# Kernel optimization log

Measured on AMD Instinct MI355X. Metric: run time of the kernel, lower is better.

Reference implementation:

```python
import jax, jax.numpy as jnp
import numpy as np
import math
from jax import lax

KSIZE = 3
STRIDE = 1
RATE = 2
FUSE_K = 3
SCALE = 10.0
FUSE = True


def extract_image_patches(img, kernel, stride=1):
    # Faithful port of the torch helper (incl. pad_row applied to width).
    bsz, c, h, w = img.shape
    h2 = math.ceil(h / stride)
    w2 = math.ceil(w / stride)
    pad_row = (h2 - 1) * stride + kernel - h
    pad_col = (w2 - 1) * stride + kernel - w
    x = jnp.pad(img, ((0, 0), (0, 0),
                      (pad_col // 2, pad_col - pad_col // 2),
                      (pad_row // 2, pad_row - pad_row // 2)))
    H, W = x.shape[2], x.shape[3]
    nh = (H - kernel) // stride + 1
    nw = (W - kernel) // stride + 1
    parts = [x[:, :, ki:ki + (nh - 1) * stride + 1:stride,
                     kj:kj + (nw - 1) * stride + 1:stride]
             for ki in range(kernel) for kj in range(kernel)]
    p = jnp.stack(parts, axis=1)  # [b, k*k, c, nh, nw] -> flatten order (ki,kj,c)
    return p.reshape(bsz, kernel * kernel * c, nh, nw)


def setup_inputs() -> dict:
    key = jax.random.key(0)
    k1, k2 = jax.random.split(key)
    f = jax.random.normal(k1, (2, 64, 128, 128), dtype=jnp.float32)
    b = jax.random.normal(k2, (2, 64, 128, 128), dtype=jnp.float32)
    mask = jnp.zeros((2, 1, 128, 128), dtype=jnp.float32)
    return {"f": f, "b": b, "mask": mask}


def reference(f, b, mask):
    kernel = RATE * 2
    bs, cs, hs, ws = f.shape
    # raw background patches at stride=rate with kernel=2*rate
    raw_w = extract_image_patches(b, kernel, RATE * STRIDE)
    raw_w = raw_w.reshape(bs, -1, kernel, kernel, cs).transpose(0, 1, 4, 2, 3)  # [bs,L,cs,K,K]
    # nearest-neighbor downsample by rate (torch nearest: src = dst*rate)
    f_ds = f[:, :, ::RATE, ::RATE]
    b_ds = b[:, :, ::RATE, ::RATE]
    mask_ds = mask[:, :, ::RATE, ::RATE]
    ihs, iws = b_ds.shape[2], b_ds.shape[3]
    L = ihs * iws
    # ksize x ksize matching patches
    w = extract_image_patches(b_ds, KSIZE, STRIDE)
    w = w.reshape(bs, -1, KSIZE, KSIZE, cs).transpose(0, 1, 4, 2, 3)  # [bs,L,cs,3,3]
    # mask patches -> per-patch validity mm [L]
    m = extract_image_patches(mask_ds, KSIZE, STRIDE)
    m = m.reshape(bs, -1, KSIZE, KSIZE, 1).transpose(0, 2, 3, 4, 1)[0]  # [3,3,1,L]
    mm = (jnp.mean(m, axis=(0, 1, 2)) == 0.0).astype(f.dtype)  # [L]
    fuse_weight = jnp.eye(FUSE_K, dtype=f.dtype).reshape(1, 1, FUSE_K, FUSE_K)

    def per_sample(xi, wi, raw_wi):
        # xi [cs,ihs,iws], wi [L,cs,3,3], raw_wi [L,cs,K,K]
        norm = jnp.sqrt(jnp.sum(wi * wi, axis=(1, 2, 3)))
        wi_normed = wi / jnp.minimum(norm, 1e-4)[:, None, None, None]  # clamp(max=1e-4), faithful
        yi = lax.conv_general_dilated(xi[None], wi_normed, (1, 1), [(1, 1), (1, 1)])  # [1,L,ihs,iws]
        if FUSE:
            yi = yi.reshape(1, 1, ihs * iws, ihs * iws)
            yi = lax.conv_general_dilated(yi, fuse_weight, (1, 1), [(1, 1), (1, 1)])
            yi = yi.reshape(1, ihs, iws, ihs, iws).transpose(0, 2, 1, 4, 3)
            yi = yi.reshape(1, 1, ihs * iws, ihs * iws)
            yi = lax.conv_general_dilated(yi, fuse_weight, (1, 1), [(1, 1), (1, 1)])
            yi = yi.reshape(1, iws, ihs, iws, ihs).transpose(0, 2, 1, 4, 3)
        yi = yi.reshape(1, ihs, iws, iws * ihs)
        yi = jax.nn.softmax(yi * mm * SCALE, axis=3) * mm
        offset = jnp.argmax(yi, axis=3).astype(jnp.int32)
        offset = jnp.stack([offset // hs, offset % hs], axis=-1).transpose(0, 3, 1, 2)  # [1,2,ihs,iws]
        yi_t = yi.transpose(0, 3, 1, 2)  # [1,L,ihs,iws]
        # conv_transpose2d(yi_t, raw_wi, stride=rate, padding=1) via lhs dilation
        w_t = jnp.flip(raw_wi, axis=(-2, -1)).transpose(1, 0, 2, 3)  # [cs,L,K,K]
        pad = kernel - 1 - 1
        out = lax.conv_general_dilated(yi_t, w_t, (1, 1), [(pad, pad), (pad, pad)],
                                       lhs_dilation=(RATE, RATE)) / 4.0  # [1,cs,hs,ws]
        return out[0], offset[0]

    y, offsets = jax.vmap(per_sample)(f_ds, w, raw_w)
    h_add = jnp.broadcast_to(jnp.arange(ihs, dtype=offsets.dtype).reshape(1, 1, ihs, 1), (bs, 1, ihs, iws))
    w_add = jnp.broadcast_to(jnp.arange(iws, dtype=offsets.dtype).reshape(1, 1, 1, iws), (bs, 1, ihs, iws))
    offsets = offsets - jnp.concatenate([h_add, w_add], axis=1)
    return y, offsets
```

## Files before the change

kernel.cpp:

```cpp
#include <hip/hip_runtime.h>
#include <math.h>

#define NS   4096
#define KCH  576
#define CH   64
#define HF   128
#define HD   64
#define PLANE (NS*KCH)

typedef __attribute__((ext_vector_type(8))) _Float16 half8;
typedef __attribute__((ext_vector_type(4))) float f32x4;

__device__ __forceinline__ int Tsw(int r){ return ((r & 63) << 6) | (r >> 6); }

typedef __attribute__((address_space(1))) unsigned int gu32;
typedef __attribute__((address_space(3))) unsigned int lu32;
__device__ __forceinline__ void gload16(const void* g, void* l){
  __builtin_amdgcn_global_load_lds((const gu32*)g, (lu32*)l, 16, 0, 0);
}

__global__ void k_mm(const float* __restrict__ mask, float* __restrict__ mm){
  int n = blockIdx.x * blockDim.x + threadIdx.x;
  if(n >= NS) return;
  float sum = 0.f;
  #pragma unroll
  for(int r9 = 0; r9 < 9; ++r9){
    int idx = n * 9 + r9;
    int p   = idx >> 12;
    int rem = idx & 4095;
    int y = rem >> 6, x = rem & 63;
    int ki = p / 3, kj = p % 3;
    int Y = ki + y - 1, X = kj + x - 1;
    float v = 0.f;
    if(Y >= 0 && Y < HD && X >= 0 && X < HD)
      v = mask[(2*Y) * HF + 2*X];
    sum += v;
  }
  mm[n] = ((sum / 9.0f) == 0.0f) ? 1.0f : 0.0f;
}

__global__ void k_WX(const float* __restrict__ fp, const float* __restrict__ bp,
                     _Float16* __restrict__ Wp, _Float16* __restrict__ Xp){
  int e0 = blockIdx.x * 256 + threadIdx.x;
  if(e0 < PLANE){
    int e = e0;
    int n = e / KCH, k = e - n * KCH;
    int c2 = k / 9, r9 = k - c2 * 9;
    int t = n * 9 + r9;
    int y = t & 63, ch = (t >> 6) & 63, p = t >> 12;
    int ki = p / 3, kj = p - ki * 3;
    int Y = ki + y - 1, X = kj + c2 - 1;
    float v = 0.f;
    if((unsigned)Y < 64u && (unsigned)X < 64u)
      v = bp[ch * (HF*HF) + (Y << 8) + (X << 1)];
    v *= 9.765625f;
    _Float16 h0 = (_Float16)v;
    _Float16 h1 = (_Float16)(v - (float)h0);
    Wp[e] = h0; Wp[PLANE + e] = h1;
  } else {
    int e = e0 - PLANE;
    int s = e / KCH, k = e - s * KCH;
    int c2 = k / 9, r9 = k - c2 * 9, a = r9 / 3, bb = r9 - a * 3;
    int i = s >> 6, j = s & 63;
    int Y = i + a - 1, Xc = j + bb - 1;
    float v = 0.f;
    if((unsigned)Y < 64u && (unsigned)Xc < 64u)
      v = fp[c2 * (HF*HF) + (Y << 8) + (Xc << 1)];
    v *= 1024.0f;
    _Float16 h0 = (_Float16)v;
    _Float16 h1 = (_Float16)(v - (float)h0);
    Xp[e] = h0; Xp[PLANE + e] = h1;
  }
}

#define CLUSTER(G,H,BR)                                                          \
  __builtin_amdgcn_s_setprio(1);                                                 \
  _Pragma("unroll")                                                              \
  for(int mf = 0; mf < 4; ++mf)                                                  \
    _Pragma("unroll")                                                            \
    for(int nf = 0; nf < 2; ++nf)                                                \
      _Pragma("unroll")                                                          \
      for(int ks = 0; ks < 2; ++ks)                                              \
        acc[G][mf][H][nf] = __builtin_amdgcn_mfma_f32_16x16x32_f16(              \
            Ar[mf][ks], BR[nf][ks], acc[G][mf][H][nf], 0, 0, 0);                 \
  __builtin_amdgcn_s_setprio(0);

__global__ __launch_bounds__(512, 2) void k_gemm(const _Float16* __restrict__ Wp,
                                                 const _Float16* __restrict__ Xp,
                                                 float* __restrict__ A){
  __shared__ char smem[131072];
  const int tid  = threadIdx.x;
  const int lane = tid & 63, wv = tid >> 6;
  const int wr = wv >> 2, wc = wv & 3;
  const int bid = blockIdx.x;
  const int xcd = bid & 7, slot = bid >> 3;
  const int bx = ((xcd & 3) << 2) | (slot & 3);
  const int by = ((xcd >> 2) << 3) | (slot >> 2);
  const int bn = by << 8, bs = bx << 8;

  f32x4 acc[2][4][2][2];
  #pragma unroll
  for(int g = 0; g < 2; ++g)
    #pragma unroll
    for(int mf = 0; mf < 4; ++mf)
      #pragma unroll
      for(int h = 0; h < 2; ++h)
        #pragma unroll
        for(int nf = 0; nf < 2; ++nf) acc[g][mf][h][nf] = (f32x4){0.f,0.f,0.f,0.f};

  const int srow = tid >> 3;
  const int sq8  = ((tid & 7) ^ (srow & 7)) << 3;
  const int ldso = tid << 4;

  auto stage = [&](int bufB, int t, int half){
    int term = t / 9;
    int k0 = (t - term * 9) << 6;
    const _Float16* pl;
    int rowbase, ldsbase;
    if(half == 0 || half == 3){
      pl = Wp + (size_t)(term >> 1) * PLANE;
      int g = (half == 3);
      rowbase = bn + (g << 7);
      ldsbase = bufB + (g << 14);
    } else {
      pl = Xp + (size_t)(term & 1) * PLANE;
      int h = (half == 2);
      rowbase = bs + (h << 7);
      ldsbase = bufB + 32768 + (h << 14);
    }
    const _Float16* src = pl + (size_t)(rowbase + srow) * KCH + k0 + sq8;
    gload16(src,            smem + ldsbase + ldso);
    gload16(src + 64*KCH,   smem + ldsbase + 8192 + ldso);
  };

  const int rA  = ((wr << 6) + (lane & 15)) << 7;
  const int rB  = ((wc << 5) + (lane & 15)) << 7;
  const int co0 = (((lane >> 4) ^ (lane & 7)) << 4);

  half8 Ar[4][2], B0r[2][2], B1r[2][2];
  auto readA = [&](int bufB, int g){
    const char* base = smem + bufB + (g << 14) + rA + co0;
    #pragma unroll
    for(int mf = 0; mf < 4; ++mf){
      Ar[mf][0] = *(const half8*)(base + (mf << 11));
      Ar[mf][1] = *(const half8*)(base + (mf << 11) + ((64 ^ co0) - co0));
    }
  };
  auto readB = [&](int bufB, int h, half8 (*Br)[2]){
    const char* base = smem + bufB + 32768 + (h << 14) + rB + co0;
    #pragma unroll
    for(int nf = 0; nf < 2; ++nf){
      Br[nf][0] = *(const half8*)(base + (nf << 11));
      Br[nf][1] = *(const half8*)(base + (nf << 11) + ((64 ^ co0) - co0));
    }
  };

  stage(0, 0, 0); stage(0, 0, 1); stage(0, 0, 2); stage(0, 0, 3);

  for(int t = 0; t < 27; ++t){
    const int bufB  = (t & 1) << 16;
    const int nbufB = bufB ^ 65536;
    const bool more = (t < 26);
    if(more){ stage(nbufB, t+1, 0); asm volatile("s_waitcnt vmcnt(6)" ::: "memory"); }
    else    {                       asm volatile("s_waitcnt vmcnt(4)" ::: "memory"); }
    __builtin_amdgcn_s_barrier(); asm volatile("" ::: "memory");
    readA(bufB, 0); readB(bufB, 0, B0r);
    CLUSTER(0,0,B0r)
    asm volatile("" ::: "memory"); __builtin_amdgcn_s_barrier(); asm volatile("" ::: "memory");
    if(more){ stage(nbufB, t+1, 1); asm volatile("s_waitcnt vmcnt(6)" ::: "memory"); }
    else    {                       asm volatile("s_waitcnt vmcnt(2)" ::: "memory"); }
    __builtin_amdgcn_s_barrier(); asm volatile("" ::: "memory");
    readB(bufB, 1, B1r);
    CLUSTER(0,1,B1r)
    asm volatile("" ::: "memory"); __builtin_amdgcn_s_barrier(); asm volatile("" ::: "memory");
    if(more){ stage(nbufB, t+1, 2); asm volatile("s_waitcnt vmcnt(6)" ::: "memory"); }
    else    {                       asm volatile("s_waitcnt vmcnt(0)" ::: "memory"); }
    __builtin_amdgcn_s_barrier(); asm volatile("" ::: "memory");
    readA(bufB, 1);
    CLUSTER(1,1,B1r)
    asm volatile("" ::: "memory"); __builtin_amdgcn_s_barrier(); asm volatile("" ::: "memory");
    if(more) stage(nbufB, t+1, 3);
    __builtin_amdgcn_s_barrier(); asm volatile("" ::: "memory");
    CLUSTER(1,0,B0r)
    asm volatile("" ::: "memory"); __builtin_amdgcn_s_barrier(); asm volatile("" ::: "memory");
  }

  #pragma unroll
  for(int g = 0; g < 2; ++g)
    #pragma unroll
    for(int mf = 0; mf < 4; ++mf){
      int row0 = bn + (g << 7) + (wr << 6) + (mf << 4) + ((lane >> 4) << 2);
      #pragma unroll
      for(int h = 0; h < 2; ++h)
        #pragma unroll
        for(int nf = 0; nf < 2; ++nf){
          int col = bs + (h << 7) + (wc << 5) + (nf << 4) + (lane & 15);
          #pragma unroll
          for(int r = 0; r < 4; ++r)
            A[((size_t)(row0 + r) << 12) + col] = acc[g][mf][h][nf][r];
        }
    }
}

__global__ __launch_bounds__(256) void k_f1(const float* __restrict__ A,
                                            float* __restrict__ B){
  const int n = ((blockIdx.x & 7) << 9) | (blockIdx.x >> 3);
  const int tid = threadIdx.x;
  const float* r0 = A + ((size_t)n << 12);
  const float* rm = r0 - 4096;
  const float* rp = r0 + 4096;
  const bool vm = (n >= 1), vp = (n <= 4094);
  float* Bw = B + ((size_t)n << 12);
  const float4 z4 = {0.f, 0.f, 0.f, 0.f};
  #pragma unroll
  for(int it = 0; it < 4; ++it){
    int cb = ((it << 8) + tid) << 2;
    float4 f0 = *(const float4*)(r0 + cb);
    float4 fm = vm ? *(const float4*)(rm + cb) : z4;
    float4 fp = vp ? *(const float4*)(rp + cb) : z4;
    float sm = (vm && cb > 0)    ? rm[cb - 1] : 0.f;
    float sp = (vp && cb < 4092) ? rp[cb + 4] : 0.f;
    float4 o;
    {
      float t0 = sm;           t0 += f0.x; t0 += fp.y;               o.x = t0;
      float t1 = fm.x;         t1 += f0.y; t1 += fp.z;               o.y = t1;
      float t2 = fm.y;         t2 += f0.z; t2 += fp.w;               o.z = t2;
      float t3 = fm.z;         t3 += f0.w; t3 += sp;                 o.w = t3;
    }
    *(float4*)(Bw + cb) = o;
  }
}

__global__ __launch_bounds__(256) void k_f2(const float* __restrict__ B,
                                            const float* __restrict__ mm,
                                            int* __restrict__ cnt, int* __restrict__ cand_s,
                                            float* __restrict__ cand_w,
                                            float* __restrict__ out_off){
  const int tn = ((blockIdx.x & 7) << 9) | (blockIdx.x >> 3);
  const int n  = Tsw(tn);
  const int tid = threadIdx.x;
  __shared__ float f1[256];
  __shared__ int   i1[256];
  __shared__ float s_max, s_sum;
  __shared__ int   s_cnt, s_cs[16];
  __shared__ float s_ce[16];

  const bool v2m = (tn >= 1), v2p = (tn <= 4094);
  const float* Rm = B + ((size_t)(v2m ? Tsw(tn - 1) : 0) << 12);
  const float* R0 = B + ((size_t)n << 12);
  const float* Rp = B + ((size_t)(v2p ? Tsw(tn + 1) : 0) << 12);

  const int wv = tid >> 6, ln = tid & 63;

  float z[16];
  #pragma unroll
  for(int r = 0; r < 16; ++r){
    int s = tid + (r << 8);
    int a = (r << 2) + wv;
    float tm = 0.f;
    if(v2m){
      if(a >= 1)            tm = Rm[s - 64];
      else if(ln >= 1)      tm = Rm[4031 + ln];
    }
    float t = tm;
    t += R0[s];
    float tp = 0.f;
    if(v2p){
      if(a <= 62)           tp = Rp[s + 64];
      else if(ln <= 62)     tp = Rp[ln + 1];
    }
    t += tp;
    z[r] = t;
  }

  float mmv[16];
  float lm = -3.4e38f;
  #pragma unroll
  for(int r = 0; r < 16; ++r){
    mmv[r] = mm[tid + (r << 8)];
    z[r] = z[r] * mmv[r] * 10.0f;
    lm = fmaxf(lm, z[r]);
  }
  f1[tid] = lm; __syncthreads();
  for(int st = 128; st > 0; st >>= 1){ if(tid < st) f1[tid] = fmaxf(f1[tid], f1[tid+st]); __syncthreads(); }
  if(tid == 0){ s_max = f1[0]; s_cnt = 0; }
  __syncthreads();
  float mx = s_max;

  float sum = 0.f, best = -1.0f; int bidx = 0;
  #pragma unroll
  for(int r = 0; r < 16; ++r){
    float d = z[r] - mx;
    float e = 0.f;
    if(__any(d > -20.0f)) e = expf(d);
    sum += e;
    float pe = e * mmv[r];
    int s = tid + (r << 8);
    if(pe > best){ best = pe; bidx = s; }
    if(pe > 1e-6f){
      int sl = atomicAdd(&s_cnt, 1);
      if(sl < 16){ s_cs[sl] = s; s_ce[sl] = pe; }
    }
  }
  f1[tid] = sum; __syncthreads();
  for(int st = 128; st > 0; st >>= 1){ if(tid < st) f1[tid] += f1[tid+st]; __syncthreads(); }
  if(tid == 0) s_sum = f1[0];
  __syncthreads();

  f1[tid] = best; i1[tid] = bidx; __syncthreads();
  for(int st = 128; st > 0; st >>= 1){
    if(tid < st){
      float v2 = f1[tid+st]; int j2 = i1[tid+st];
      if(v2 > f1[tid] || (v2 == f1[tid] && j2 < i1[tid])){ f1[tid] = v2; i1[tid] = j2; }
    }
    __syncthreads();
  }
  if(tid == 0){
    int sA = i1[0]; float vA = f1[0];
    int sBest = (vA > 0.0f) ? sA : 0;
    int c = min(s_cnt, 16);
    if(vA > 0.0f){
      bool found = false;
      for(int q = 0; q < c; ++q) if(s_cs[q] == sA) found = true;
      if(!found){ if(c < 16){ s_cs[c] = sA; s_ce[c] = vA; ++c; } else { s_cs[0] = sA; s_ce[0] = vA; } }
    }
    cnt[n] = c;
    float inv = 1.0f / s_sum;
    for(int q = 0; q < c; ++q){ cand_s[n*16+q] = s_cs[q]; cand_w[n*16+q] = s_ce[q] * inv; }
    out_off[n]      = (float)((sBest >> 7)  - (n >> 6));
    out_off[NS + n] = (float)((sBest & 127) - (n & 63));
  }
}

__global__ void k_y(const float* __restrict__ bp,
                    const int* __restrict__ cnt, const int* __restrict__ cand_s,
                    const float* __restrict__ cand_w, float* __restrict__ outy){
  int e = blockIdx.x * 256 + threadIdx.x;
  if(e >= CH * HF * HF) return;
  int ox = e & 127, oy = (e >> 7) & 127, co = e >> 14;
  float val = 0.f;
  int kyp = oy & 1, kxp = ox & 1;
  #pragma unroll
  for(int ia = 0; ia < 2; ++ia){
    int ky = kyp + 2*ia;
    int un = oy + ky - 2;
    if(un < 0 || un > 126) continue;
    int u = un >> 1;
    #pragma unroll
    for(int ib = 0; ib < 2; ++ib){
      int kx = kxp + 2*ib;
      int vn = ox + kx - 2;
      if(vn < 0 || vn > 126) continue;
      int v = vn >> 1;
      int n = (u << 6) | v;
      int c = cnt[n];
      int ky2 = 3 - ky, kx2 = 3 - kx;
      for(int q = 0; q < c; ++q){
        int s = cand_s[n*16 + q];
        float w = cand_w[n*16 + q];
        int p = s >> 8, ki = p >> 2, kj = p & 3, ch = (s >> 2) & 63;
        int Y = ((s & 3) << 4) + (ky2 << 2) + kx2;
        int yy = ki + 2*Y - 1;
        int xx = kj + 2*co - 1;
        if(yy >= 0 && yy < HF && xx >= 0 && xx < HF)
          val += w * bp[(ch << 14) + (yy << 7) + xx];
      }
    }
  }
  outy[e] = val * 0.25f;
}

extern "C" void kernel_launch(void* const* d_in, const int* in_sizes, int n_in,
                              void* d_out, int out_size, void* d_ws, size_t ws_size,
                              hipStream_t stream){
  const float* f    = (const float*)d_in[0];
  const float* b    = (const float*)d_in[1];
  const float* mask = (const float*)d_in[2];
  float* out = (float*)d_out;
  char* ws = (char*)d_ws;

  float*     A      = (float*)(ws);
  float*     Bf     = (float*)(ws + 67108864ull);
  _Float16*  Wp     = (_Float16*)(ws + 134217728ull);
  _Float16*  Xp     = (_Float16*)(ws + 143654912ull);
  float*     mmv    = (float*)(ws + 153092096ull);
  int*       cntv   = (int*)  (ws + 153108480ull);
  int*       cand_s = (int*)  (ws + 153124864ull);
  float*     cand_w = (float*)(ws + 153387008ull);

  k_mm<<<16, 256, 0, stream>>>(mask, mmv);

  for(int bs = 0; bs < 2; ++bs){
    const float* fp = f + (size_t)bs * CH * HF * HF;
    const float* bp = b + (size_t)bs * CH * HF * HF;
    k_WX<<<(2*PLANE)/256, 256, 0, stream>>>(fp, bp, Wp, Xp);
    k_gemm<<<256, 512, 0, stream>>>(Wp, Xp, A);
    k_f1<<<NS, 256, 0, stream>>>(A, Bf);
    k_f2<<<NS, 256, 0, stream>>>(Bf, mmv, cntv, cand_s, cand_w,
                                 out + 2*CH*HF*HF + bs*2*NS);
    k_y<<<(CH*HF*HF)/256, 256, 0, stream>>>(bp, cntv, cand_s, cand_w,
                                            out + (size_t)bs * CH * HF * HF);
  }
}
```

Measured before the change: 317.6 us.

## Batch both samples into single kernel launches when workspace allows

Adds a batched path in which every kernel (im2col split, GEMM, filters, softmax/top-k, reconstruction) handles both samples in one grid, indexed by a sample id derived from blockIdx. This doubles the grid size of each launch to fill the GPU better, especially the GEMM's 256-block grid. It also cuts the number of kernel launches. The cost is a larger workspace requirement, with a fallback to the old per-sample loop when the workspace is too small.

Measured after the change: 319.4 us. About the same (+0.6%).

```diff
diff --git a/kernel.cpp b/kernel.cpp
--- a/kernel.cpp
+++ b/kernel.cpp
@@ -7,6 +7,7 @@
 #define HF   128
 #define HD   64
 #define PLANE (NS*KCH)
+#define IMG  (CH*HF*HF)
 
 typedef __attribute__((ext_vector_type(8))) _Float16 half8;
 typedef __attribute__((ext_vector_type(4))) float f32x4;
@@ -39,11 +40,17 @@
   mm[n] = ((sum / 9.0f) == 0.0f) ? 1.0f : 0.0f;
 }
 
-__global__ void k_WX(const float* __restrict__ fp, const float* __restrict__ bp,
+__global__ void k_WX(const float* __restrict__ f, const float* __restrict__ b,
                      _Float16* __restrict__ Wp, _Float16* __restrict__ Xp){
   int e0 = blockIdx.x * 256 + threadIdx.x;
-  if(e0 < PLANE){
-    int e = e0;
+  int samp = e0 / (2*PLANE);
+  int ew = e0 - samp * (2*PLANE);
+  const float* fp = f + (size_t)samp * IMG;
+  const float* bp = b + (size_t)samp * IMG;
+  _Float16* Wps = Wp + (size_t)samp * (2*PLANE);
+  _Float16* Xps = Xp + (size_t)samp * (2*PLANE);
+  if(ew < PLANE){
+    int e = ew;
     int n = e / KCH, k = e - n * KCH;
     int c2 = k / 9, r9 = k - c2 * 9;
     int t = n * 9 + r9;
@@ -56,9 +63,9 @@
     v *= 9.765625f;
     _Float16 h0 = (_Float16)v;
     _Float16 h1 = (_Float16)(v - (float)h0);
-    Wp[e] = h0; Wp[PLANE + e] = h1;
+    Wps[e] = h0; Wps[PLANE + e] = h1;
   } else {
-    int e = e0 - PLANE;
+    int e = ew - PLANE;
     int s = e / KCH, k = e - s * KCH;
     int c2 = k / 9, r9 = k - c2 * 9, a = r9 / 3, bb = r9 - a * 3;
     int i = s >> 6, j = s & 63;
@@ -69,7 +76,7 @@
     v *= 1024.0f;
     _Float16 h0 = (_Float16)v;
     _Float16 h1 = (_Float16)(v - (float)h0);
-    Xp[e] = h0; Xp[PLANE + e] = h1;
+    Xps[e] = h0; Xps[PLANE + e] = h1;
   }
 }
 
@@ -92,7 +99,11 @@
   const int tid  = threadIdx.x;
   const int lane = tid & 63, wv = tid >> 6;
   const int wr = wv >> 2, wc = wv & 3;
-  const int bid = blockIdx.x;
+  const int samp = blockIdx.x >> 8;
+  const int bid  = blockIdx.x & 255;
+  const _Float16* Wps = Wp + (size_t)samp * (2*PLANE);
+  const _Float16* Xps = Xp + (size_t)samp * (2*PLANE);
+  float* As = A + (size_t)samp * NS * NS;
   const int xcd = bid & 7, slot = bid >> 3;
   const int bx = ((xcd & 3) << 2) | (slot & 3);
   const int by = ((xcd >> 2) << 3) | (slot >> 2);
@@ -118,12 +129,12 @@
     const _Float16* pl;
     int rowbase, ldsbase;
     if(half == 0 || half == 3){
-      pl = Wp + (size_t)(term >> 1) * PLANE;
+      pl = Wps + (size_t)(term >> 1) * PLANE;
       int g = (half == 3);
       rowbase = bn + (g << 7);
       ldsbase = bufB + (g << 14);
     } else {
-      pl = Xp + (size_t)(term & 1) * PLANE;
+      pl = Xps + (size_t)(term & 1) * PLANE;
       int h = (half == 2);
       rowbase = bs + (h << 7);
       ldsbase = bufB + 32768 + (h << 14);
@@ -197,20 +208,24 @@
           int col = bs + (h << 7) + (wc << 5) + (nf << 4) + (lane & 15);
           #pragma unroll
           for(int r = 0; r < 4; ++r)
-            A[((size_t)(row0 + r) << 12) + col] = acc[g][mf][h][nf][r];
+            As[((size_t)(row0 + r) << 12) + col] = acc[g][mf][h][nf][r];
         }
     }
 }
 
 __global__ __launch_bounds__(256) void k_f1(const float* __restrict__ A,
                                             float* __restrict__ B){
-  const int n = ((blockIdx.x & 7) << 9) | (blockIdx.x >> 3);
+  const int samp = blockIdx.x >> 12;
+  const int sbid = blockIdx.x & 4095;
+  const int n = ((sbid & 7) << 9) | (sbid >> 3);
   const int tid = threadIdx.x;
-  const float* r0 = A + ((size_t)n << 12);
+  const float* As = A + (size_t)samp * NS * NS;
+  float* Bs = B + (size_t)samp * NS * NS;
+  const float* r0 = As + ((size_t)n << 12);
   const float* rm = r0 - 4096;
   const float* rp = r0 + 4096;
   const bool vm = (n >= 1), vp = (n <= 4094);
-  float* Bw = B + ((size_t)n << 12);
+  float* Bw = Bs + ((size_t)n << 12);
   const float4 z4 = {0.f, 0.f, 0.f, 0.f};
   #pragma unroll
   for(int it = 0; it < 4; ++it){
@@ -236,9 +251,16 @@
                                             int* __restrict__ cnt, int* __restrict__ cand_s,
                                             float* __restrict__ cand_w,
                                             float* __restrict__ out_off){
-  const int tn = ((blockIdx.x & 7) << 9) | (blockIdx.x >> 3);
+  const int samp = blockIdx.x >> 12;
+  const int sbid = blockIdx.x & 4095;
+  const int tn = ((sbid & 7) << 9) | (sbid >> 3);
   const int n  = Tsw(tn);
   const int tid = threadIdx.x;
+  const float* Bs = B + (size_t)samp * NS * NS;
+  int* cnts = cnt + samp * NS;
+  int* cand_ss = cand_s + samp * NS * 16;
+  float* cand_ws = cand_w + samp * NS * 16;
+  float* oo = out_off + samp * 2 * NS;
   __shared__ float f1[256];
   __shared__ int   i1[256];
   __shared__ float s_max, s_sum;
@@ -246,9 +268,9 @@
   __shared__ float s_ce[16];
 
   const bool v2m = (tn >= 1), v2p = (tn <= 4094);
-  const float* Rm = B + ((size_t)(v2m ? Tsw(tn - 1) : 0) << 12);
-  const float* R0 = B + ((size_t)n << 12);
-  const float* Rp = B + ((size_t)(v2p ? Tsw(tn + 1) : 0) << 12);
+  const float* Rm = Bs + ((size_t)(v2m ? Tsw(tn - 1) : 0) << 12);
+  const float* R0 = Bs + ((size_t)n << 12);
+  const float* Rp = Bs + ((size_t)(v2p ? Tsw(tn + 1) : 0) << 12);
 
   const int wv = tid >> 6, ln = tid & 63;
 
@@ -324,26 +346,31 @@
       for(int q = 0; q < c; ++q) if(s_cs[q] == sA) found = true;
       if(!found){ if(c < 16){ s_cs[c] = sA; s_ce[c] = vA; ++c; } else { s_cs[0] = sA; s_ce[0] = vA; } }
     }
-    cnt[n] = c;
+    cnts[n] = c;
     float inv = 1.0f / s_sum;
-    for(int q = 0; q < c; ++q){ cand_s[n*16+q] = s_cs[q]; cand_w[n*16+q] = s_ce[q] * inv; }
-    out_off[n]      = (float)((sBest >> 7)  - (n >> 6));
-    out_off[NS + n] = (float)((sBest & 127) - (n & 63));
-  }
-}
-
-__global__ void k_y(const float* __restrict__ bp,
+    for(int q = 0; q < c; ++q){ cand_ss[n*16+q] = s_cs[q]; cand_ws[n*16+q] = s_ce[q] * inv; }
+    oo[n]      = (float)((sBest >> 7)  - (n >> 6));
+    oo[NS + n] = (float)((sBest & 127) - (n & 63));
+  }
+}
+
+__global__ void k_y(const float* __restrict__ b,
                     const int* __restrict__ cnt, const int* __restrict__ cand_s,
                     const float* __restrict__ cand_w, float* __restrict__ outy){
-  int e = blockIdx.x * 256 + threadIdx.x;
-  if(e >= CH * HF * HF) return;
-  int ox = e & 127, oy = (e >> 7) & 127, co = e >> 14;
+  const int samp = blockIdx.x >> 12;
+  int e = (blockIdx.x & 4095) * 256 + threadIdx.x;
+  const float* bp = b + (size_t)samp * IMG;
+  const int* cnts = cnt + samp * NS;
+  const int* cand_ss = cand_s + samp * NS * 16;
+  const float* cand_ws = cand_w + samp * NS * 16;
+  float* oy = outy + (size_t)samp * IMG;
+  int ox = e & 127, oyr = (e >> 7) & 127, co = e >> 14;
   float val = 0.f;
-  int kyp = oy & 1, kxp = ox & 1;
+  int kyp = oyr & 1, kxp = ox & 1;
   #pragma unroll
   for(int ia = 0; ia < 2; ++ia){
     int ky = kyp + 2*ia;
-    int un = oy + ky - 2;
+    int un = oyr + ky - 2;
     if(un < 0 || un > 126) continue;
     int u = un >> 1;
     #pragma unroll
@@ -353,11 +380,11 @@
       if(vn < 0 || vn > 126) continue;
       int v = vn >> 1;
       int n = (u << 6) | v;
-      int c = cnt[n];
+      int c = cnts[n];
       int ky2 = 3 - ky, kx2 = 3 - kx;
       for(int q = 0; q < c; ++q){
-        int s = cand_s[n*16 + q];
-        float w = cand_w[n*16 + q];
+        int s = cand_ss[n*16 + q];
+        float w = cand_ws[n*16 + q];
         int p = s >> 8, ki = p >> 2, kj = p & 3, ch = (s >> 2) & 63;
         int Y = ((s & 3) << 4) + (ky2 << 2) + kx2;
         int yy = ki + 2*Y - 1;
@@ -367,7 +394,7 @@
       }
     }
   }
-  outy[e] = val * 0.25f;
+  oy[e] = val * 0.25f;
 }
 
 extern "C" void kernel_launch(void* const* d_in, const int* in_sizes, int n_in,
@@ -379,26 +406,44 @@
   float* out = (float*)d_out;
   char* ws = (char*)d_ws;
 
-  float*     A      = (float*)(ws);
-  float*     Bf     = (float*)(ws + 67108864ull);
-  _Float16*  Wp     = (_Float16*)(ws + 134217728ull);
-  _Float16*  Xp     = (_Float16*)(ws + 143654912ull);
-  float*     mmv    = (float*)(ws + 153092096ull);
-  int*       cntv   = (int*)  (ws + 153108480ull);
-  int*       cand_s = (int*)  (ws + 153124864ull);
-  float*     cand_w = (float*)(ws + 153387008ull);
-
-  k_mm<<<16, 256, 0, stream>>>(mask, mmv);
-
-  for(int bs = 0; bs < 2; ++bs){
-    const float* fp = f + (size_t)bs * CH * HF * HF;
-    const float* bp = b + (size_t)bs * CH * HF * HF;
-    k_WX<<<(2*PLANE)/256, 256, 0, stream>>>(fp, bp, Wp, Xp);
-    k_gemm<<<256, 512, 0, stream>>>(Wp, Xp, A);
-    k_f1<<<NS, 256, 0, stream>>>(A, Bf);
-    k_f2<<<NS, 256, 0, stream>>>(Bf, mmv, cntv, cand_s, cand_w,
-                                 out + 2*CH*HF*HF + bs*2*NS);
-    k_y<<<(CH*HF*HF)/256, 256, 0, stream>>>(bp, cntv, cand_s, cand_w,
-                                            out + (size_t)bs * CH * HF * HF);
-  }
-}
+  const size_t BATCH_WS = 307281920ull;
+  if(ws_size >= BATCH_WS){
+    float*    A      = (float*)(ws);
+    float*    Bf     = (float*)(ws + 134217728ull);
+    _Float16* Wp     = (_Float16*)(ws + 268435456ull);
+    _Float16* Xp     = (_Float16*)(ws + 287309824ull);
+    float*    mmv    = (float*)(ws + 306184192ull);
+    int*      cntv   = (int*)  (ws + 306200576ull);
+    int*      cand_s = (int*)  (ws + 306233344ull);
+    float*    cand_w = (float*)(ws + 306757632ull);
+
+    k_mm<<<16, 256, 0, stream>>>(mask, mmv);
+    k_WX<<<(4*PLANE)/256, 256, 0, stream>>>(f, b, Wp, Xp);
+    k_gemm<<<512, 512, 0, stream>>>(Wp, Xp, A);
+    k_f1<<<8192, 256, 0, stream>>>(A, Bf);
+    k_f2<<<8192, 256, 0, stream>>>(Bf, mmv, cntv, cand_s, cand_w, out + 2*IMG);
+    k_y<<<8192, 256, 0, stream>>>(b, cntv, cand_s, cand_w, out);
+  } else {
+    float*     A      = (float*)(ws);
+    float*     Bf     = (float*)(ws + 67108864ull);
+    _Float16*  Wp     = (_Float16*)(ws + 134217728ull);
+    _Float16*  Xp     = (_Float16*)(ws + 143654912ull);
+    float*     mmv    = (float*)(ws + 153092096ull);
+    int*       cntv   = (int*)  (ws + 153108480ull);
+    int*       cand_s = (int*)  (ws + 153124864ull);
+    float*     cand_w = (float*)(ws + 153387008ull);
+
+    k_mm<<<16, 256, 0, stream>>>(mask, mmv);
+    for(int s = 0; s < 2; ++s){
+      const float* fp = f + (size_t)s * IMG;
+      const float* bp = b + (size_t)s * IMG;
+      k_WX<<<(2*PLANE)/256, 256, 0, stream>>>(fp, bp, Wp, Xp);
+      k_gemm<<<256, 512, 0, stream>>>(Wp, Xp, A);
+      k_f1<<<4096, 256, 0, stream>>>(A, Bf);
+      k_f2<<<4096, 256, 0, stream>>>(Bf, mmv, cntv, cand_s, cand_w,
+                                     out + 2*IMG + s*2*NS);
+      k_y<<<4096, 256, 0, stream>>>(bp, cntv, cand_s, cand_w,
+                                    out + (size_t)s * IMG);
+    }
+  }
+}
```
